# Optimization experiments

Hardware: AMD Instinct MI355X
Metric: run time of the kernel (lower is better)

Reference implementation:

```python
import jax, jax.numpy as jnp
import numpy as np

N_MODELS = 16
IN_F = 1024
OUT_F = 1024
N_TOK = 8192


def setup_inputs() -> dict:
    key = jax.random.key(0)
    k1, k2, k3, k4 = jax.random.split(key, 4)
    x = jax.random.normal(k1, (N_TOK, IN_F), dtype=jnp.float32)
    idxs = jax.random.randint(k2, (N_TOK,), 0, N_MODELS, dtype=jnp.int64)
    w = jax.random.normal(k3, (N_MODELS, IN_F, OUT_F), dtype=jnp.float32) * 0.02
    b = jax.random.normal(k4, (N_MODELS, OUT_F), dtype=jnp.float32) * 0.02
    return {"x": x, "idxs": idxs, "w": w, "b": b}


def reference(x, idxs, w, b):
    # Equivalent math to the torch loop: for each expert i, tokens with
    # idxs==i get x @ w[i] + b[i]; finally ReLU over all outputs.
    # Loop over the small fixed expert count; selection by mask avoids
    # materializing the [N, E, out] tensor or gathering per-token weights.
    y = jnp.zeros((x.shape[0], w.shape[2]), dtype=x.dtype)
    for i in range(w.shape[0]):
        yi = x @ w[i] + b[i]  # [N, out]
        y = jnp.where((idxs == i)[:, None], yi, y)
    return jax.nn.relu(y)
```

## Files before the change

kernel.cpp:

```cpp
#include <hip/hip_runtime.h>
#include <hip/hip_bf16.h>
#include <stdint.h>

#define N_MODELS 16
#define IN_F 1024
#define OUT_F 1024
#define N_TOK 8192
#define MAX_MT 80
#define READY_MAGIC 0x1F2E3D4C

typedef unsigned short u16;
using us4   = __attribute__((ext_vector_type(4))) unsigned short;
using s16x8 = __attribute__((ext_vector_type(8))) short;
using f32x4 = __attribute__((ext_vector_type(4))) float;

__device__ __forceinline__ u16 f2bf(float f) {
    union { float f; uint32_t u; } v;
    v.f = f;
    uint32_t u = v.u;
    u += 0x7fffu + ((u >> 16) & 1u);
    return (u16)(u >> 16);
}

__device__ __forceinline__ void gload16(const u16* g, u16* l) {
    __builtin_amdgcn_global_load_lds(
        (const __attribute__((address_space(1))) void*)g,
        (__attribute__((address_space(3))) void*)l, 16, 0, 0);
}

#define ROW 17
#define WBLOCKS 2048
#define XBLOCKS (MAX_MT * 8)

__global__ __launch_bounds__(256)
void prep_kernel(const float* __restrict__ w, const float* __restrict__ x,
                 const int* __restrict__ idxs,
                 int* __restrict__ perm,
                 int* __restrict__ offs,
                 int* __restrict__ tile_off,
                 u16* __restrict__ wT, u16* __restrict__ xg,
                 int* __restrict__ ready)
{
    int t  = threadIdx.x;
    int bx = blockIdx.x;

    if (bx == 0) {
        __shared__ int cnt[256 * ROW];
        __shared__ int offsS[N_MODELS + 1];
#pragma unroll
        for (int e = 0; e < N_MODELS; ++e) cnt[t * ROW + e] = 0;
        __syncthreads();

        int base = t * 32;
#pragma unroll
        for (int i = 0; i < 32; ++i) cnt[t * ROW + idxs[base + i]] += 1;
        __syncthreads();

#pragma unroll
        for (int s = 1; s < 256; s <<= 1) {
            int v[N_MODELS];
#pragma unroll
            for (int e = 0; e < N_MODELS; ++e)
                v[e] = (t >= s) ? cnt[(t - s) * ROW + e] : 0;
            __syncthreads();
#pragma unroll
            for (int e = 0; e < N_MODELS; ++e)
                cnt[t * ROW + e] += v[e];
            __syncthreads();
        }

        if (t == 0) {
            int o = 0, to = 0;
            for (int e = 0; e < N_MODELS; ++e) {
                int c = cnt[255 * ROW + e];
                offsS[e] = o;
                offs[e] = o; tile_off[e] = to;
                to += (c + 127) >> 7;
                o  += c;
            }
            offsS[N_MODELS] = o;
            offs[N_MODELS] = o; tile_off[N_MODELS] = to;
        }
        __syncthreads();

        int cur[N_MODELS];
#pragma unroll
        for (int e = 0; e < N_MODELS; ++e)
            cur[e] = offsS[e] + ((t > 0) ? cnt[(t - 1) * ROW + e] : 0);
        __syncthreads();
#pragma unroll
        for (int e = 0; e < N_MODELS; ++e) cnt[t * ROW + e] = cur[e];

#pragma unroll
        for (int i = 0; i < 32; ++i) {
            int tok = base + i;
            int e = idxs[tok];
            perm[cnt[t * ROW + e]++] = tok;
        }
        __syncthreads();
        if (t == 0)
            __hip_atomic_store(ready, READY_MAGIC, __ATOMIC_RELEASE, __HIP_MEMORY_SCOPE_AGENT);
        return;
    }

    if (bx <= WBLOCKS) {
        int wb = bx - 1;
        int e  = wb >> 7;
        int nt = (wb >> 4) & 7;
        int kg = wb & 15;
        int n    = t & 127;
        int half = t >> 7;

        const float* wp = w  + (size_t)e * (IN_F * OUT_F) + (size_t)nt * 128 + n;
        u16*         ob = wT + ((size_t)(e * 8 + nt)) * 131072 + (size_t)n * 8;

#pragma unroll
        for (int i = 0; i < 4; ++i) {
            int kog = kg * 8 + half + i * 2;
            float r[8];
#pragma unroll
            for (int j = 0; j < 8; ++j)
                r[j] = wp[(size_t)(kog * 8 + j) * OUT_F];
            union { __hip_bfloat162 h; uint32_t u; } c0, c1, c2, c3;
            c0.h = __float22bfloat162_rn(make_float2(r[0], r[1]));
            c1.h = __float22bfloat162_rn(make_float2(r[2], r[3]));
            c2.h = __float22bfloat162_rn(make_float2(r[4], r[5]));
            c3.h = __float22bfloat162_rn(make_float2(r[6], r[7]));
            union { s16x8 v; uint32_t u[4]; } outv;
            outv.u[0] = c0.u; outv.u[1] = c1.u; outv.u[2] = c2.u; outv.u[3] = c3.u;
            *(s16x8*)(ob + (size_t)kog * 1024) = outv.v;
        }
        return;
    }

    __shared__ int gate;
    if (t == 0) {
        while (__hip_atomic_load(ready, __ATOMIC_RELAXED, __HIP_MEMORY_SCOPE_AGENT) != READY_MAGIC) {}
        (void)__hip_atomic_load(ready, __ATOMIC_ACQUIRE, __HIP_MEMORY_SCOPE_AGENT);
        gate = 1;
    }
    __syncthreads();
    (void)gate;

    int bx2 = bx - (WBLOCKS + 1);
    int mt = bx2 >> 3;
    int kg = bx2 & 7;
    int total = tile_off[N_MODELS];
    if (mt >= total) return;
    int e = 0;
    while (tile_off[e + 1] <= mt) ++e;
    int s0   = offs[e] + (mt - tile_off[e]) * 128;
    int sEnd = offs[e + 1];

    int r0   = t >> 3;
    int apos = t & 7;
    int q    = apos >> 1;
    int j0   = (apos & 1) * 4;

    int toks[4];
#pragma unroll
    for (int i = 0; i < 4; ++i) {
        int r = r0 + i * 32;
        toks[i] = (s0 + r < sEnd) ? perm[s0 + r] : -1;
    }

    u16* outx = xg + (size_t)mt * 131072;
#pragma unroll
    for (int kb4 = 0; kb4 < 4; ++kb4) {
        int kb = kg * 4 + kb4;
        int k  = kb * 32 + apos * 4;
#pragma unroll
        for (int i = 0; i < 4; ++i) {
            int r = r0 + i * 32;
            float4 v;
            if (toks[i] >= 0) v = *(const float4*)(x + (size_t)toks[i] * IN_F + k);
            else              v = make_float4(0.f, 0.f, 0.f, 0.f);
            us4 pk; pk.x = f2bf(v.x); pk.y = f2bf(v.y); pk.z = f2bf(v.z); pk.w = f2bf(v.w);
            *(us4*)(outx + (size_t)kb * 4096 + (size_t)q * 1024 + r * 8 + j0) = pk;
        }
    }
}

__global__ __launch_bounds__(256, 3)
void gemm_kernel(const u16* __restrict__ xg, const u16* __restrict__ wT,
                 const float* __restrict__ bias,
                 const int* __restrict__ perm, const int* __restrict__ offs,
                 const int* __restrict__ tile_off,
                 float* __restrict__ out)
{
    __shared__ u16 Bs[2][8192];
    __shared__ int   permS[128];
    __shared__ float biasS[128];
    __shared__ int   toS[N_MODELS + 1];

    int t = threadIdx.x;
    int o    = blockIdx.x;
    int wgid = (o & 7) * MAX_MT + (o >> 3);
    int bt   = wgid >> 3;
    int nt   = wgid & 7;

    if (t <= N_MODELS) toS[t] = tile_off[t];
    __syncthreads();
    if (bt >= toS[N_MODELS]) return;

    int e = 0;
    while (toS[e + 1] <= bt) ++e;
    int s0   = offs[e] + (bt - toS[e]) * 128;
    int sEnd = offs[e + 1];
    int mValid = sEnd - s0; if (mValid > 128) mValid = 128;

    if (t < 128) {
        permS[t] = (s0 + t < sEnd) ? perm[s0 + t] : 0;
        biasS[t] = bias[(size_t)e * OUT_F + nt * 128 + t];
    }

    const u16* atile = xg + (size_t)bt * 131072;
    const u16* btile = wT + ((size_t)(e * 8 + nt)) * 131072;

    int lane = t & 63;
    int wv   = t >> 6;
    int wm   = (wv >> 1) * 64;
    int wn   = (wv & 1) * 64;
    int m    = lane & 15;
    int q    = lane >> 4;

    int aoff = q * 1024 + (wm + m) * 8;
    int boff = q * 1024 + (wn + m) * 8;

    f32x4 acc[4][4];
#pragma unroll
    for (int i = 0; i < 4; ++i)
#pragma unroll
        for (int j = 0; j < 4; ++j)
            acc[i][j] = (f32x4){0.f, 0.f, 0.f, 0.f};

#pragma unroll
    for (int i = 0; i < 4; ++i)
        gload16(btile + wv * 2048 + i * 512 + lane * 8, &Bs[0][wv * 2048 + i * 512]);

    s16x8 a0[4], a1[4];
#pragma unroll
    for (int mt2 = 0; mt2 < 4; ++mt2)
        a0[mt2] = *(const s16x8*)(atile + aoff + mt2 * 128);
#pragma unroll
    for (int mt2 = 0; mt2 < 4; ++mt2)
        a1[mt2] = *(const s16x8*)(atile + 4096 + aoff + mt2 * 128);

    for (int kb2 = 0; kb2 < 16; ++kb2) {
        int cur = kb2 & 1;
        __syncthreads();
        if (kb2 < 15) {
            const u16* gb = btile + (size_t)(kb2 + 1) * 8192;
#pragma unroll
            for (int i = 0; i < 4; ++i)
                gload16(gb + wv * 2048 + i * 512 + lane * 8,
                        &Bs[cur ^ 1][wv * 2048 + i * 512]);
        }
        if (kb2 > 0) {
#pragma unroll
            for (int mt2 = 0; mt2 < 4; ++mt2)
                a1[mt2] = *(const s16x8*)(atile + (size_t)kb2 * 8192 + 4096 + aoff + mt2 * 128);
        }

        s16x8 bf[4];
#pragma unroll
        for (int nt2 = 0; nt2 < 4; ++nt2)
            bf[nt2] = *(const s16x8*)(&Bs[cur][boff + nt2 * 128]);
#pragma unroll
        for (int mt2 = 0; mt2 < 4; ++mt2)
#pragma unroll
            for (int nt2 = 0; nt2 < 4; ++nt2)
                acc[mt2][nt2] = __builtin_amdgcn_mfma_f32_16x16x32_bf16(
                    a0[mt2], bf[nt2], acc[mt2][nt2], 0, 0, 0);

        if (kb2 < 15) {
#pragma unroll
            for (int mt2 = 0; mt2 < 4; ++mt2)
                a0[mt2] = *(const s16x8*)(atile + (size_t)(kb2 + 1) * 8192 + aoff + mt2 * 128);
        }

#pragma unroll
        for (int nt2 = 0; nt2 < 4; ++nt2)
            bf[nt2] = *(const s16x8*)(&Bs[cur][4096 + boff + nt2 * 128]);
#pragma unroll
        for (int mt2 = 0; mt2 < 4; ++mt2)
#pragma unroll
            for (int nt2 = 0; nt2 < 4; ++nt2)
                acc[mt2][nt2] = __builtin_amdgcn_mfma_f32_16x16x32_bf16(
                    a1[mt2], bf[nt2], acc[mt2][nt2], 0, 0, 0);
    }

#pragma unroll
    for (int mt2 = 0; mt2 < 4; ++mt2) {
        int rbase = wm + mt2 * 16 + q * 4;
#pragma unroll
        for (int i = 0; i < 4; ++i) {
            int r = rbase + i;
            if (r < mValid) {
                int tok = permS[r];
                float* orow = out + (size_t)tok * OUT_F + nt * 128;
#pragma unroll
                for (int nt2 = 0; nt2 < 4; ++nt2) {
                    int col = wn + nt2 * 16 + m;
                    float v = acc[mt2][nt2][i] + biasS[col];
                    orow[col] = v > 0.f ? v : 0.f;
                }
            }
        }
    }
}

extern "C" void kernel_launch(void* const* d_in, const int* in_sizes, int n_in,
                              void* d_out, int out_size, void* d_ws, size_t ws_size,
                              hipStream_t stream) {
    const float* x    = (const float*)d_in[0];
    const int*   idxs = (const int*)d_in[1];
    const float* w    = (const float*)d_in[2];
    const float* b    = (const float*)d_in[3];
    float* out = (float*)d_out;

    u16* wT = (u16*)d_ws;
    u16* xg = wT + (size_t)N_MODELS * IN_F * OUT_F;
    int* perm     = (int*)(xg + (size_t)MAX_MT * 32 * 4096);
    int* offs     = perm + N_TOK;
    int* tile_off = offs + (N_MODELS + 1);
    int* ready    = tile_off + (N_MODELS + 1);

    prep_kernel<<<1 + WBLOCKS + XBLOCKS, 256, 0, stream>>>(
        w, x, idxs, perm, offs, tile_off, wT, xg, ready);
    gemm_kernel<<<8 * MAX_MT, 256, 0, stream>>>(xg, wT, b, perm, offs, tile_off, out);
}
```

Before: 186.3 us.

## Replace spin-wait gate with per-block redundant histogram and scatter-based x packing

Drops the global ready flag and spin-wait that made the x-packing blocks wait for block 0's permutation. Instead, each x-packing block recomputes the expert histogram and prefix scan in shared memory. It then works out destination slots for its own 128 consecutive tokens and scatters them into the tiled bf16 buffer. Reads of x become contiguous while writes become scattered. Every block now repeats the histogram and scan work, and padded tile rows are no longer zeroed.

```diff
diff --git a/kernel.cpp b/kernel.cpp
--- a/kernel.cpp
+++ b/kernel.cpp
@@ -7,7 +7,6 @@
 #define OUT_F 1024
 #define N_TOK 8192
 #define MAX_MT 80
-#define READY_MAGIC 0x1F2E3D4C
 
 typedef unsigned short u16;
 using us4   = __attribute__((ext_vector_type(4))) unsigned short;
@@ -30,7 +29,7 @@
 
 #define ROW 17
 #define WBLOCKS 2048
-#define XBLOCKS (MAX_MT * 8)
+#define XBLOCKS2 512
 
 __global__ __launch_bounds__(256)
 void prep_kernel(const float* __restrict__ w, const float* __restrict__ x,
@@ -38,15 +37,16 @@
                  int* __restrict__ perm,
                  int* __restrict__ offs,
                  int* __restrict__ tile_off,
-                 u16* __restrict__ wT, u16* __restrict__ xg,
-                 int* __restrict__ ready)
+                 u16* __restrict__ wT, u16* __restrict__ xg)
 {
+    __shared__ int cnt[256 * ROW];
+    __shared__ int offsS[N_MODELS + 1];
+    __shared__ int tileS[N_MODELS + 1];
+    __shared__ int destS[128];
     int t  = threadIdx.x;
     int bx = blockIdx.x;
 
     if (bx == 0) {
-        __shared__ int cnt[256 * ROW];
-        __shared__ int offsS[N_MODELS + 1];
 #pragma unroll
         for (int e = 0; e < N_MODELS; ++e) cnt[t * ROW + e] = 0;
         __syncthreads();
@@ -97,9 +97,6 @@
             int e = idxs[tok];
             perm[cnt[t * ROW + e]++] = tok;
         }
-        __syncthreads();
-        if (t == 0)
-            __hip_atomic_store(ready, READY_MAGIC, __ATOMIC_RELEASE, __HIP_MEMORY_SCOPE_AGENT);
         return;
     }
 
@@ -133,50 +130,73 @@
         return;
     }
 
-    __shared__ int gate;
+    int bx2 = bx - (WBLOCKS + 1);
+    int g   = bx2 >> 3;
+    int kg  = bx2 & 7;
+
+#pragma unroll
+    for (int e = 0; e < N_MODELS; ++e) cnt[t * ROW + e] = 0;
+    __syncthreads();
+
+    int base = t * 32;
+#pragma unroll
+    for (int i = 0; i < 32; ++i) cnt[t * ROW + idxs[base + i]] += 1;
+    __syncthreads();
+
+#pragma unroll
+    for (int s = 1; s < 256; s <<= 1) {
+        int v[N_MODELS];
+#pragma unroll
+        for (int e = 0; e < N_MODELS; ++e)
+            v[e] = (t >= s) ? cnt[(t - s) * ROW + e] : 0;
+        __syncthreads();
+#pragma unroll
+        for (int e = 0; e < N_MODELS; ++e)
+            cnt[t * ROW + e] += v[e];
+        __syncthreads();
+    }
+
     if (t == 0) {
-        while (__hip_atomic_load(ready, __ATOMIC_RELAXED, __HIP_MEMORY_SCOPE_AGENT) != READY_MAGIC) {}
-        (void)__hip_atomic_load(ready, __ATOMIC_ACQUIRE, __HIP_MEMORY_SCOPE_AGENT);
-        gate = 1;
-    }
-    __syncthreads();
-    (void)gate;
-
-    int bx2 = bx - (WBLOCKS + 1);
-    int mt = bx2 >> 3;
-    int kg = bx2 & 7;
-    int total = tile_off[N_MODELS];
-    if (mt >= total) return;
-    int e = 0;
-    while (tile_off[e + 1] <= mt) ++e;
-    int s0   = offs[e] + (mt - tile_off[e]) * 128;
-    int sEnd = offs[e + 1];
+        int to = 0;
+        for (int e = 0; e < N_MODELS; ++e) {
+            tileS[e] = to;
+            to += (cnt[255 * ROW + e] + 127) >> 7;
+        }
+    }
+    __syncthreads();
+
+    if (t < 4) {
+        int tr = g * 4 + t;
+        int curL[N_MODELS];
+#pragma unroll
+        for (int e = 0; e < N_MODELS; ++e)
+            curL[e] = (tr > 0) ? cnt[(tr - 1) * ROW + e] : 0;
+        for (int i = 0; i < 32; ++i) {
+            int tok = tr * 32 + i;
+            int e = idxs[tok];
+            destS[t * 32 + i] = (tileS[e] << 7) + curL[e]++;
+        }
+    }
+    __syncthreads();
 
     int r0   = t >> 3;
     int apos = t & 7;
     int q    = apos >> 1;
     int j0   = (apos & 1) * 4;
 
-    int toks[4];
-#pragma unroll
-    for (int i = 0; i < 4; ++i) {
-        int r = r0 + i * 32;
-        toks[i] = (s0 + r < sEnd) ? perm[s0 + r] : -1;
-    }
-
-    u16* outx = xg + (size_t)mt * 131072;
 #pragma unroll
     for (int kb4 = 0; kb4 < 4; ++kb4) {
         int kb = kg * 4 + kb4;
         int k  = kb * 32 + apos * 4;
 #pragma unroll
         for (int i = 0; i < 4; ++i) {
-            int r = r0 + i * 32;
-            float4 v;
-            if (toks[i] >= 0) v = *(const float4*)(x + (size_t)toks[i] * IN_F + k);
-            else              v = make_float4(0.f, 0.f, 0.f, 0.f);
+            int lt  = r0 + i * 32;
+            int tok = g * 128 + lt;
+            int d   = destS[lt];
+            const float4 v = *(const float4*)(x + (size_t)tok * IN_F + k);
             us4 pk; pk.x = f2bf(v.x); pk.y = f2bf(v.y); pk.z = f2bf(v.z); pk.w = f2bf(v.w);
-            *(us4*)(outx + (size_t)kb * 4096 + (size_t)q * 1024 + r * 8 + j0) = pk;
+            *(us4*)(xg + (size_t)(d >> 7) * 131072 + (size_t)kb * 4096
+                       + (size_t)q * 1024 + (d & 127) * 8 + j0) = pk;
         }
     }
 }
@@ -324,9 +344,8 @@
     int* perm     = (int*)(xg + (size_t)MAX_MT * 32 * 4096);
     int* offs     = perm + N_TOK;
     int* tile_off = offs + (N_MODELS + 1);
-    int* ready    = tile_off + (N_MODELS + 1);
-
-    prep_kernel<<<1 + WBLOCKS + XBLOCKS, 256, 0, stream>>>(
-        w, x, idxs, perm, offs, tile_off, wT, xg, ready);
+
+    prep_kernel<<<1 + WBLOCKS + XBLOCKS2, 256, 0, stream>>>(
+        w, x, idxs, perm, offs, tile_off, wT, xg);
     gemm_kernel<<<8 * MAX_MT, 256, 0, stream>>>(xg, wT, b, perm, offs, tile_off, out);
 }
```

Result: slower. 199.2 us (+6.9%).
